# Performance work log

Measured on AMD Instinct MI355X. Metric: run time of the kernel, lower is better.

The kernel has to match this reference:

```python
import jax, jax.numpy as jnp
import numpy as np

HIDDEN = 1024
N_HEADS = 16
HEAD_DIM = HIDDEN // N_HEADS
WINDOW = 256  # symmetric window: keys j with i - W//2 <= j <= i + W//2
BATCH, SEQ = 2, 2048


def setup_inputs() -> dict:
    key = jax.random.key(0)
    ks = jax.random.split(key, 9)
    s = 0.02
    return {
        "x":  jax.random.normal(ks[0], (BATCH, SEQ, HIDDEN), dtype=jnp.float32),
        "wq": jax.random.normal(ks[1], (HIDDEN, HIDDEN), dtype=jnp.float32) * s,
        "bq": jnp.zeros((HIDDEN,), dtype=jnp.float32),
        "wk": jax.random.normal(ks[2], (HIDDEN, HIDDEN), dtype=jnp.float32) * s,
        "bk": jnp.zeros((HIDDEN,), dtype=jnp.float32),
        "wv": jax.random.normal(ks[3], (HIDDEN, HIDDEN), dtype=jnp.float32) * s,
        "bv": jnp.zeros((HIDDEN,), dtype=jnp.float32),
        "wo": jax.random.normal(ks[4], (HIDDEN, HIDDEN), dtype=jnp.float32) * s,
        "bo": jnp.zeros((HIDDEN,), dtype=jnp.float32),
    }


def reference(x, wq, bq, wk, bk, wv, bv, wo, bo):
    B, S, Hs = x.shape
    scale = HEAD_DIM ** -0.5

    def proj(w, b):
        # [B,S,Hs] -> [B,H,S,D]
        return (x @ w + b).reshape(B, S, N_HEADS, HEAD_DIM).transpose(0, 2, 1, 3)

    q = proj(wq, bq)
    k = proj(wk, bk)
    v = proj(wv, bv)

    # Clipped sliding window == band-masked full attention (identical softmax weights).
    scores = jnp.einsum('bhid,bhjd->bhij', q, k) * scale  # [B,H,S,S]
    i = jnp.arange(S)[:, None]
    j = jnp.arange(S)[None, :]
    band = (j >= i - WINDOW // 2) & (j <= i + WINDOW // 2)
    scores = jnp.where(band, scores, -jnp.inf)
    attn = jax.nn.softmax(scores, axis=-1)
    out = jnp.einsum('bhij,bhjd->bhid', attn, v)  # [B,H,S,D]
    out = out.transpose(0, 2, 1, 3).reshape(B, S, Hs)
    return out @ wo + bo
```

## Files before the change

kernel.cpp:

```cpp
#include <hip/hip_runtime.h>
#include <hip/hip_bf16.h>
#include <stdint.h>

#define BATCH 2
#define SEQ   2048
#define HID   1024
#define NH    16
#define HD    64
#define W2    128

using bhalf8 = __attribute__((ext_vector_type(8))) short;
using fvec4  = __attribute__((ext_vector_type(4))) float;
using u16x8  = __attribute__((ext_vector_type(8))) unsigned short;

__device__ __forceinline__ unsigned short f2bf(float f) {
    union { float f; unsigned int u; } c; c.f = f;
    unsigned int u = c.u;
    u += 0x7FFFu + ((u >> 16) & 1u);
    return (unsigned short)(u >> 16);
}

__device__ __forceinline__ fvec4 zero4() {
    fvec4 z = {0.f, 0.f, 0.f, 0.f};
    return z;
}

__device__ __forceinline__ void load_lds16(const void* g, void* l) {
    __builtin_amdgcn_global_load_lds(
        (const __attribute__((address_space(1))) void*)g,
        (__attribute__((address_space(3))) void*)l, 16, 0, 0);
}

__device__ __forceinline__ float rowmax16(float v) {
    v = fmaxf(v, __shfl_xor(v, 1));
    v = fmaxf(v, __shfl_xor(v, 2));
    v = fmaxf(v, __shfl_xor(v, 4));
    v = fmaxf(v, __shfl_xor(v, 8));
    return v;
}
__device__ __forceinline__ float rowsum16(float v) {
    v += __shfl_xor(v, 1);
    v += __shfl_xor(v, 2);
    v += __shfl_xor(v, 4);
    v += __shfl_xor(v, 8);
    return v;
}


__global__ __launch_bounds__(256) void k_convert_x(const float* __restrict__ x,
                                                   unsigned short* __restrict__ xb) {
    int i = (blockIdx.x * 256 + threadIdx.x) * 8;
    float4 a = *(const float4*)(x + i);
    float4 b = *(const float4*)(x + i + 4);
    u16x8 o;
    o[0] = f2bf(a.x); o[1] = f2bf(a.y); o[2] = f2bf(a.z); o[3] = f2bf(a.w);
    o[4] = f2bf(b.x); o[5] = f2bf(b.y); o[6] = f2bf(b.z); o[7] = f2bf(b.w);
    *(u16x8*)(xb + i) = o;
}

__global__ __launch_bounds__(256) void k_transpose_w(
    const float* __restrict__ w0, const float* __restrict__ w1,
    const float* __restrict__ w2, const float* __restrict__ w3,
    unsigned short* __restrict__ t0, unsigned short* __restrict__ t1,
    unsigned short* __restrict__ t2, unsigned short* __restrict__ t3) {
    int z = blockIdx.z;
    const float* src = (z == 0) ? w0 : (z == 1) ? w1 : (z == 2) ? w2 : w3;
    unsigned short* dst = (z == 0) ? t0 : (z == 1) ? t1 : (z == 2) ? t2 : t3;
    __shared__ float tile[32][33];
    int n0 = blockIdx.x * 32, k0 = blockIdx.y * 32;
    int tx = threadIdx.x, ty = threadIdx.y;
#pragma unroll
    for (int r = 0; r < 4; ++r)
        tile[ty + 8 * r][tx] = src[(size_t)(k0 + ty + 8 * r) * HID + n0 + tx];
    __syncthreads();
#pragma unroll
    for (int r = 0; r < 4; ++r)
        dst[(size_t)(n0 + ty + 8 * r) * HID + k0 + tx] = f2bf(tile[tx][ty + 8 * r]);
}


__device__ __forceinline__ void stage_tile64(const unsigned short* __restrict__ A,
                                             const unsigned short* __restrict__ Bt,
                                             int m0, int n0, int k0,
                                             unsigned short* As, unsigned short* Bs,
                                             int t) {
#pragma unroll
    for (int i = 0; i < 2; ++i) {
        int chunk = t + 512 * i;
        int row = chunk >> 3, ch = chunk & 7;
        int chs = ch ^ (row & 7);
        load_lds16(A + (size_t)(m0 + row) * HID + k0 + chs * 8, As + chunk * 8);
        load_lds16(Bt + (size_t)(n0 + row) * HID + k0 + chs * 8, Bs + chunk * 8);
    }
}

__device__ __forceinline__ void gemm_tile8(const unsigned short* __restrict__ A,
                                           const unsigned short* __restrict__ Bt,
                                           int m0, int n0,
                                           unsigned short* As, unsigned short* Bs,
                                           fvec4 acc[4][2]) {
    const int t = threadIdx.x;
    const int lane = t & 63;
    const int wid = t >> 6;
    const int wr = wid >> 2, wc = wid & 3;
    const int c16 = lane & 15, g = lane >> 4;

#pragma unroll
    for (int mi = 0; mi < 4; ++mi)
#pragma unroll
        for (int ni = 0; ni < 2; ++ni) acc[mi][ni] = zero4();

    stage_tile64(A, Bt, m0, n0, 0, As, Bs, t);

    int cur = 0;
    for (int k0 = 0; k0 < HID; k0 += 64) {
        asm volatile("s_waitcnt vmcnt(0)" ::: "memory");
        __builtin_amdgcn_sched_barrier(0);
        __builtin_amdgcn_s_barrier();

        if (k0 + 64 < HID)
            stage_tile64(A, Bt, m0, n0, k0 + 64,
                         As + (cur ^ 1) * 8192, Bs + (cur ^ 1) * 8192, t);

        const unsigned short* Ab = As + cur * 8192;
        const unsigned short* Bb = Bs + cur * 8192;
        bhalf8 af[2][4], bf[2][2];
#pragma unroll
        for (int ks = 0; ks < 2; ++ks) {
#pragma unroll
            for (int i = 0; i < 4; ++i) {
                int ra = wr * 64 + i * 16 + c16;
                af[ks][i] = *(const bhalf8*)(Ab + ra * 64 + ((4 * ks + g) ^ (ra & 7)) * 8);
            }
#pragma unroll
            for (int i = 0; i < 2; ++i) {
                int rb = wc * 32 + i * 16 + c16;
                bf[ks][i] = *(const bhalf8*)(Bb + rb * 64 + ((4 * ks + g) ^ (rb & 7)) * 8);
            }
        }
        __builtin_amdgcn_s_setprio(1);
#pragma unroll
        for (int ks = 0; ks < 2; ++ks)
#pragma unroll
            for (int mi = 0; mi < 4; ++mi)
#pragma unroll
                for (int ni = 0; ni < 2; ++ni)
                    acc[mi][ni] = __builtin_amdgcn_mfma_f32_16x16x32_bf16(
                        af[ks][mi], bf[ks][ni], acc[mi][ni], 0, 0, 0);
        __builtin_amdgcn_s_setprio(0);
        cur ^= 1;
    }
}

__global__ __launch_bounds__(512, 4) void k_gemm_qkv(
    const unsigned short* __restrict__ xb,
    const unsigned short* __restrict__ wqt, const unsigned short* __restrict__ wkt,
    const unsigned short* __restrict__ wvt,
    const float* __restrict__ bq, const float* __restrict__ bk, const float* __restrict__ bv,
    unsigned short* __restrict__ qb, unsigned short* __restrict__ kbuf,
    unsigned short* __restrict__ vt) {
    __shared__ unsigned short SH[2][2 * 128 * 64];
    const int z = blockIdx.z;
    const unsigned short* Bt = (z == 0) ? wqt : (z == 1) ? wkt : wvt;
    const float* bias = (z == 0) ? bq : (z == 1) ? bk : bv;
    const int m0 = blockIdx.y * 128, n0 = blockIdx.x * 128;
    fvec4 acc[4][2];
    gemm_tile8(xb, Bt, m0, n0, SH[0], SH[1], acc);

    const int t = threadIdx.x, lane = t & 63, wid = t >> 6;
    const int wr = wid >> 2, wc = wid & 3, c16 = lane & 15, g = lane >> 4;

    if (z != 2) {
#pragma unroll
        for (int mi = 0; mi < 4; ++mi) {
#pragma unroll
            for (int ni = 0; ni < 2; ++ni) {
                int gcol = n0 + wc * 32 + ni * 16 + c16;
                int h = gcol >> 6, d = gcol & 63;
                float bsv = bias[gcol];
#pragma unroll
                for (int r = 0; r < 4; ++r) {
                    int grow = m0 + wr * 64 + mi * 16 + 4 * g + r;
                    int b = grow >> 11, s = grow & (SEQ - 1);
                    float v = acc[mi][ni][r] + bsv;
                    if (z == 0)
                        qb[((size_t)(b * NH + h) * SEQ + s) * HD + d] = f2bf(v * 0.125f);
                    else
                        kbuf[((size_t)(b * NH + h) * SEQ + s) * HD + d] = f2bf(v);
                }
            }
        }
    } else {
        unsigned short* VL = &SH[0][0];
        __syncthreads();
#pragma unroll
        for (int mi = 0; mi < 4; ++mi)
#pragma unroll
            for (int ni = 0; ni < 2; ++ni) {
                int dl = wc * 32 + ni * 16 + c16;
                float bsv = bias[n0 + dl];
#pragma unroll
                for (int r = 0; r < 4; ++r) {
                    int sl = wr * 64 + mi * 16 + 4 * g + r;
                    VL[dl * 132 + sl] = f2bf(acc[mi][ni][r] + bsv);
                }
            }
        __syncthreads();
        const int b = m0 >> 11, sbase = m0 & (SEQ - 1);
#pragma unroll
        for (int it = 0; it < 4; ++it) {
            int slot = t + 512 * it;
            int dl = slot >> 4, ch = slot & 15;
            int gcol = n0 + dl;
            int h = gcol >> 6, d = gcol & 63;
            u16x8 v = *(const u16x8*)(VL + dl * 132 + ch * 8);
            *(u16x8*)(vt + ((size_t)(b * NH + h) * HD + d) * SEQ + sbase + ch * 8) = v;
        }
    }
}

__global__ __launch_bounds__(512, 4) void k_gemm_out(
    const unsigned short* __restrict__ attn, const unsigned short* __restrict__ wot,
    const float* __restrict__ bo, float* __restrict__ out) {
    __shared__ unsigned short SH[2][2 * 128 * 64];
    const int m0 = blockIdx.y * 128, n0 = blockIdx.x * 128;
    fvec4 acc[4][2];
    gemm_tile8(attn, wot, m0, n0, SH[0], SH[1], acc);

    const int lane = threadIdx.x & 63, wid = threadIdx.x >> 6;
    const int wr = wid >> 2, wc = wid & 3, c16 = lane & 15, g = lane >> 4;
#pragma unroll
    for (int mi = 0; mi < 4; ++mi) {
#pragma unroll
        for (int ni = 0; ni < 2; ++ni) {
            int gcol = n0 + wc * 32 + ni * 16 + c16;
            float bsv = bo[gcol];
#pragma unroll
            for (int r = 0; r < 4; ++r) {
                int grow = m0 + wr * 64 + mi * 16 + 4 * g + r;
                out[(size_t)grow * HID + gcol] = acc[mi][ni][r] + bsv;
            }
        }
    }
}

__global__ __launch_bounds__(256) void k_attn(
    const unsigned short* __restrict__ qb, const unsigned short* __restrict__ kbuf,
    const unsigned short* __restrict__ vt, unsigned short* __restrict__ attn) {
    const int bh = blockIdx.y;
    const int wid = threadIdx.x >> 6, lane = threadIdx.x & 63;
    const int g = lane >> 4, c16 = lane & 15;
    const int q0 = blockIdx.x * 64 + wid * 16;

    const unsigned short* Qp = qb + (size_t)bh * SEQ * HD;
    const unsigned short* Kp = kbuf + (size_t)bh * SEQ * HD;
    const unsigned short* Vp = vt + (size_t)bh * HD * SEQ;

    __shared__ unsigned short Plds[4][16 * 32];
    unsigned short* myP = Plds[wid];

    bhalf8 qf0, qf1;
    {
        const unsigned short* p = Qp + (size_t)(q0 + c16) * HD + g * 8;
        qf0 = *(const bhalf8*)p;
        qf1 = *(const bhalf8*)(p + 32);
    }
    fvec4 acc[4];
#pragma unroll
    for (int i = 0; i < 4; ++i) acc[i] = zero4();
    float mrow[4] = {-1e30f, -1e30f, -1e30f, -1e30f};
    float srow[4] = {0.f, 0.f, 0.f, 0.f};

    int kstart = q0 - W2; if (kstart < 0) kstart = 0; kstart &= ~31;
    int kend = q0 + 15 + W2; if (kend > SEQ - 1) kend = SEQ - 1;

    for (int t0 = kstart; t0 <= kend; t0 += 32) {
        fvec4 sc0 = zero4(), sc1 = zero4();
        {
            const unsigned short* kp = Kp + (size_t)(t0 + c16) * HD + g * 8;
            bhalf8 ka = *(const bhalf8*)kp;
            bhalf8 kb2 = *(const bhalf8*)(kp + 32);
            sc0 = __builtin_amdgcn_mfma_f32_16x16x32_bf16(qf0, ka, sc0, 0, 0, 0);
            sc0 = __builtin_amdgcn_mfma_f32_16x16x32_bf16(qf1, kb2, sc0, 0, 0, 0);
        }
        {
            const unsigned short* kp = Kp + (size_t)(t0 + 16 + c16) * HD + g * 8;
            bhalf8 ka = *(const bhalf8*)kp;
            bhalf8 kb2 = *(const bhalf8*)(kp + 32);
            sc1 = __builtin_amdgcn_mfma_f32_16x16x32_bf16(qf0, ka, sc1, 0, 0, 0);
            sc1 = __builtin_amdgcn_mfma_f32_16x16x32_bf16(qf1, kb2, sc1, 0, 0, 0);
        }
#pragma unroll
        for (int r = 0; r < 4; ++r) {
            int ia = q0 + 4 * g + r;
            int j0 = t0 + c16, j1 = t0 + 16 + c16;
            if (j0 < ia - W2 || j0 > ia + W2) sc0[r] = -1e30f;
            if (j1 < ia - W2 || j1 > ia + W2) sc1[r] = -1e30f;
        }
#pragma unroll
        for (int r = 0; r < 4; ++r) {
            float pm = rowmax16(fmaxf(sc0[r], sc1[r]));
            float mn = fmaxf(mrow[r], pm);
            float f = __expf(mrow[r] - mn);
            mrow[r] = mn;
            float p0 = __expf(sc0[r] - mn);
            float p1 = __expf(sc1[r] - mn);
            srow[r] = srow[r] * f + (p0 + p1);
#pragma unroll
            for (int db = 0; db < 4; ++db) acc[db][r] *= f;
            myP[(4 * g + r) * 32 + c16] = f2bf(p0);
            myP[(4 * g + r) * 32 + 16 + c16] = f2bf(p1);
        }
        asm volatile("s_waitcnt lgkmcnt(0)" ::: "memory");
        __builtin_amdgcn_sched_barrier(0);
        bhalf8 pf = *(const bhalf8*)(myP + c16 * 32 + g * 8);
#pragma unroll
        for (int db = 0; db < 4; ++db) {
            const unsigned short* vp = Vp + (size_t)(db * 16 + c16) * SEQ + t0 + g * 8;
            bhalf8 vf = *(const bhalf8*)vp;
            acc[db] = __builtin_amdgcn_mfma_f32_16x16x32_bf16(pf, vf, acc[db], 0, 0, 0);
        }
    }

    float inv[4];
#pragma unroll
    for (int r = 0; r < 4; ++r) inv[r] = 1.f / rowsum16(srow[r]);

    const int b = bh >> 4, h = bh & 15;
#pragma unroll
    for (int db = 0; db < 4; ++db)
#pragma unroll
        for (int r = 0; r < 4; ++r) {
            int si = q0 + 4 * g + r;
            attn[((size_t)(b * SEQ) + si) * HID + h * HD + db * 16 + c16] =
                f2bf(acc[db][r] * inv[r]);
        }
}


extern "C" void kernel_launch(void* const* d_in, const int* in_sizes, int n_in,
                              void* d_out, int out_size, void* d_ws, size_t ws_size,
                              hipStream_t stream) {
    const float* x  = (const float*)d_in[0];
    const float* wq = (const float*)d_in[1];
    const float* bq = (const float*)d_in[2];
    const float* wk = (const float*)d_in[3];
    const float* bk = (const float*)d_in[4];
    const float* wv = (const float*)d_in[5];
    const float* bv = (const float*)d_in[6];
    const float* wo = (const float*)d_in[7];
    const float* bo = (const float*)d_in[8];
    float* out = (float*)d_out;

    char* ws = (char*)d_ws;
    unsigned short* xb   = (unsigned short*)(ws);
    unsigned short* wqt  = (unsigned short*)(ws + (8u << 20));
    unsigned short* wkt  = wqt + 1024 * 1024;
    unsigned short* wvt  = wkt + 1024 * 1024;
    unsigned short* wot  = wvt + 1024 * 1024;
    unsigned short* qb   = wot + 1024 * 1024;
    unsigned short* kbuf = qb + 4u * 1024 * 1024;
    unsigned short* vt   = kbuf + 4u * 1024 * 1024;
    unsigned short* attn = vt + 4u * 1024 * 1024;

    k_convert_x<<<dim3(2048), dim3(256), 0, stream>>>(x, xb);
    k_transpose_w<<<dim3(32, 32, 4), dim3(32, 8), 0, stream>>>(wq, wk, wv, wo,
                                                               wqt, wkt, wvt, wot);
    k_gemm_qkv<<<dim3(8, 32, 3), dim3(512), 0, stream>>>(xb, wqt, wkt, wvt,
                                                         bq, bk, bv, qb, kbuf, vt);
    k_attn<<<dim3(SEQ / 64, BATCH * NH), dim3(256), 0, stream>>>(qb, kbuf, vt, attn);
    k_gemm_out<<<dim3(8, 32), dim3(512), 0, stream>>>(attn, wot, bo, out);
}
```

Baseline: 180.4 us.

## Compute transposed attention scores to keep per-query softmax in-lane and drop LDS

Swaps the MFMA operand order so each lane holds scores for a single query column, reducing the per-row softmax reductions to two cross-group shuffles instead of four per row. The P matrix is repacked into the PV MFMA operand layout with register shuffles rather than an LDS round-trip with a waitcnt barrier. The output is then computed transposed (d by query), so stores write 4 consecutive dims per lane. The cost is more shuffles per tile, and the output store pattern changes.

```diff
diff --git a/kernel.cpp b/kernel.cpp
--- a/kernel.cpp
+++ b/kernel.cpp
@@ -29,21 +29,6 @@
     __builtin_amdgcn_global_load_lds(
         (const __attribute__((address_space(1))) void*)g,
         (__attribute__((address_space(3))) void*)l, 16, 0, 0);
-}
-
-__device__ __forceinline__ float rowmax16(float v) {
-    v = fmaxf(v, __shfl_xor(v, 1));
-    v = fmaxf(v, __shfl_xor(v, 2));
-    v = fmaxf(v, __shfl_xor(v, 4));
-    v = fmaxf(v, __shfl_xor(v, 8));
-    return v;
-}
-__device__ __forceinline__ float rowsum16(float v) {
-    v += __shfl_xor(v, 1);
-    v += __shfl_xor(v, 2);
-    v += __shfl_xor(v, 4);
-    v += __shfl_xor(v, 8);
-    return v;
 }
 
 
@@ -256,9 +241,6 @@
     const unsigned short* Kp = kbuf + (size_t)bh * SEQ * HD;
     const unsigned short* Vp = vt + (size_t)bh * HD * SEQ;
 
-    __shared__ unsigned short Plds[4][16 * 32];
-    unsigned short* myP = Plds[wid];
-
     bhalf8 qf0, qf1;
     {
         const unsigned short* p = Qp + (size_t)(q0 + c16) * HD + g * 8;
@@ -268,72 +250,95 @@
     fvec4 acc[4];
 #pragma unroll
     for (int i = 0; i < 4; ++i) acc[i] = zero4();
-    float mrow[4] = {-1e30f, -1e30f, -1e30f, -1e30f};
-    float srow[4] = {0.f, 0.f, 0.f, 0.f};
-
+    float mq = -1e30f;
+    float sq = 0.f;
+
+    const int ia = q0 + c16;
     int kstart = q0 - W2; if (kstart < 0) kstart = 0; kstart &= ~31;
     int kend = q0 + 15 + W2; if (kend > SEQ - 1) kend = SEQ - 1;
 
+    const int sl1 = ((2 * g) & 3) * 16 + c16;
+    const int sl2 = ((2 * g + 1) & 3) * 16 + c16;
+
     for (int t0 = kstart; t0 <= kend; t0 += 32) {
-        fvec4 sc0 = zero4(), sc1 = zero4();
+        fvec4 st0 = zero4(), st1 = zero4();
         {
             const unsigned short* kp = Kp + (size_t)(t0 + c16) * HD + g * 8;
             bhalf8 ka = *(const bhalf8*)kp;
-            bhalf8 kb2 = *(const bhalf8*)(kp + 32);
-            sc0 = __builtin_amdgcn_mfma_f32_16x16x32_bf16(qf0, ka, sc0, 0, 0, 0);
-            sc0 = __builtin_amdgcn_mfma_f32_16x16x32_bf16(qf1, kb2, sc0, 0, 0, 0);
+            bhalf8 ka2 = *(const bhalf8*)(kp + 32);
+            st0 = __builtin_amdgcn_mfma_f32_16x16x32_bf16(ka, qf0, st0, 0, 0, 0);
+            st0 = __builtin_amdgcn_mfma_f32_16x16x32_bf16(ka2, qf1, st0, 0, 0, 0);
         }
         {
             const unsigned short* kp = Kp + (size_t)(t0 + 16 + c16) * HD + g * 8;
-            bhalf8 ka = *(const bhalf8*)kp;
+            bhalf8 kb = *(const bhalf8*)kp;
             bhalf8 kb2 = *(const bhalf8*)(kp + 32);
-            sc1 = __builtin_amdgcn_mfma_f32_16x16x32_bf16(qf0, ka, sc1, 0, 0, 0);
-            sc1 = __builtin_amdgcn_mfma_f32_16x16x32_bf16(qf1, kb2, sc1, 0, 0, 0);
+            st1 = __builtin_amdgcn_mfma_f32_16x16x32_bf16(kb, qf0, st1, 0, 0, 0);
+            st1 = __builtin_amdgcn_mfma_f32_16x16x32_bf16(kb2, qf1, st1, 0, 0, 0);
         }
 #pragma unroll
         for (int r = 0; r < 4; ++r) {
-            int ia = q0 + 4 * g + r;
-            int j0 = t0 + c16, j1 = t0 + 16 + c16;
-            if (j0 < ia - W2 || j0 > ia + W2) sc0[r] = -1e30f;
-            if (j1 < ia - W2 || j1 > ia + W2) sc1[r] = -1e30f;
-        }
+            int j0 = t0 + 4 * g + r, j1 = j0 + 16;
+            if (j0 < ia - W2 || j0 > ia + W2) st0[r] = -1e30f;
+            if (j1 < ia - W2 || j1 > ia + W2) st1[r] = -1e30f;
+        }
+        float pm = fmaxf(fmaxf(fmaxf(st0[0], st0[1]), fmaxf(st0[2], st0[3])),
+                         fmaxf(fmaxf(st1[0], st1[1]), fmaxf(st1[2], st1[3])));
+        pm = fmaxf(pm, __shfl_xor(pm, 16));
+        pm = fmaxf(pm, __shfl_xor(pm, 32));
+        float mn = fmaxf(mq, pm);
+        float f = __expf(mq - mn);
+        mq = mn;
+        float p0[4], p1[4];
+        float psum = 0.f;
 #pragma unroll
         for (int r = 0; r < 4; ++r) {
-            float pm = rowmax16(fmaxf(sc0[r], sc1[r]));
-            float mn = fmaxf(mrow[r], pm);
-            float f = __expf(mrow[r] - mn);
-            mrow[r] = mn;
-            float p0 = __expf(sc0[r] - mn);
-            float p1 = __expf(sc1[r] - mn);
-            srow[r] = srow[r] * f + (p0 + p1);
-#pragma unroll
-            for (int db = 0; db < 4; ++db) acc[db][r] *= f;
-            myP[(4 * g + r) * 32 + c16] = f2bf(p0);
-            myP[(4 * g + r) * 32 + 16 + c16] = f2bf(p1);
-        }
-        asm volatile("s_waitcnt lgkmcnt(0)" ::: "memory");
-        __builtin_amdgcn_sched_barrier(0);
-        bhalf8 pf = *(const bhalf8*)(myP + c16 * 32 + g * 8);
+            p0[r] = __expf(st0[r] - mn);
+            p1[r] = __expf(st1[r] - mn);
+            psum += p0[r] + p1[r];
+        }
+        sq = sq * f + psum;
+#pragma unroll
+        for (int db = 0; db < 4; ++db) acc[db] *= f;
+
+        unsigned int a01 = (unsigned int)f2bf(p0[0]) | ((unsigned int)f2bf(p0[1]) << 16);
+        unsigned int a23 = (unsigned int)f2bf(p0[2]) | ((unsigned int)f2bf(p0[3]) << 16);
+        unsigned int b01 = (unsigned int)f2bf(p1[0]) | ((unsigned int)f2bf(p1[1]) << 16);
+        unsigned int b23 = (unsigned int)f2bf(p1[2]) | ((unsigned int)f2bf(p1[3]) << 16);
+        unsigned int A01 = (unsigned int)__shfl((int)a01, sl1);
+        unsigned int A23 = (unsigned int)__shfl((int)a23, sl1);
+        unsigned int A01b = (unsigned int)__shfl((int)a01, sl2);
+        unsigned int A23b = (unsigned int)__shfl((int)a23, sl2);
+        unsigned int B01 = (unsigned int)__shfl((int)b01, sl1);
+        unsigned int B23 = (unsigned int)__shfl((int)b23, sl1);
+        unsigned int B01b = (unsigned int)__shfl((int)b01, sl2);
+        unsigned int B23b = (unsigned int)__shfl((int)b23, sl2);
+        union { unsigned int u[4]; bhalf8 v; } pb;
+        pb.u[0] = (g < 2) ? A01 : B01;
+        pb.u[1] = (g < 2) ? A23 : B23;
+        pb.u[2] = (g < 2) ? A01b : B01b;
+        pb.u[3] = (g < 2) ? A23b : B23b;
+
 #pragma unroll
         for (int db = 0; db < 4; ++db) {
             const unsigned short* vp = Vp + (size_t)(db * 16 + c16) * SEQ + t0 + g * 8;
             bhalf8 vf = *(const bhalf8*)vp;
-            acc[db] = __builtin_amdgcn_mfma_f32_16x16x32_bf16(pf, vf, acc[db], 0, 0, 0);
-        }
-    }
-
-    float inv[4];
-#pragma unroll
-    for (int r = 0; r < 4; ++r) inv[r] = 1.f / rowsum16(srow[r]);
+            acc[db] = __builtin_amdgcn_mfma_f32_16x16x32_bf16(vf, pb.v, acc[db], 0, 0, 0);
+        }
+    }
+
+    sq += __shfl_xor(sq, 16);
+    sq += __shfl_xor(sq, 32);
+    float inv = 1.f / sq;
 
     const int b = bh >> 4, h = bh & 15;
+    const int si = q0 + c16;
 #pragma unroll
     for (int db = 0; db < 4; ++db)
 #pragma unroll
         for (int r = 0; r < 4; ++r) {
-            int si = q0 + 4 * g + r;
-            attn[((size_t)(b * SEQ) + si) * HID + h * HD + db * 16 + c16] =
-                f2bf(acc[db][r] * inv[r]);
+            int d = db * 16 + 4 * g + r;
+            attn[((size_t)(b * SEQ) + si) * HID + h * HD + d] = f2bf(acc[db][r] * inv);
         }
 }
 
```

Result: no change. 177.4 us (-1.7%).
